# Optimization experiments

Hardware: AMD Instinct MI355X
Metric: run time of the kernel (lower is better)

The kernel has to match this reference:

```python
import jax, jax.numpy as jnp
import numpy as np

IN_F, OUT_F, GRID = 1024, 1024, 8
B = 8192
GRID_LO, GRID_HI = -1.0, 1.0


def setup_inputs() -> dict:
    key = jax.random.key(0)
    k1, k2 = jax.random.split(key)
    x = jax.random.normal(k1, (B, IN_F), dtype=jnp.float32)
    # buffers: grid is linspace expanded over in_features; sigma = 1.5*h
    h = (GRID_HI - GRID_LO) / (GRID - 1)
    grid = jnp.broadcast_to(jnp.linspace(GRID_LO, GRID_HI, GRID, dtype=jnp.float32), (IN_F, GRID))
    sigma = jnp.float32(1.5 * h)
    # params
    scale_base = jnp.ones((IN_F, OUT_F), dtype=jnp.float32)
    scale_spline = jnp.ones((IN_F, OUT_F), dtype=jnp.float32)
    # kaiming_uniform-ish init: bound = sqrt(6/fan_in)/sqrt(1+a^2) approximated by small uniform
    fan_in = IN_F * GRID
    gain = np.sqrt(2.0 / (1.0 + 5.0 * 0.1 * 0.1))
    bound = gain * np.sqrt(3.0 / fan_in)
    spline_weight = jax.random.uniform(k2, (OUT_F, IN_F, GRID), dtype=jnp.float32, minval=-bound, maxval=bound)
    return {"x": x, "scale_base": scale_base, "spline_weight": spline_weight,
            "scale_spline": scale_spline, "grid": grid, "sigma": sigma}


def reference(x, scale_base, spline_weight, scale_spline, grid, sigma):
    # x: [B, I]; grid: [I, G]; spline_weight: [O, I, G]; scales: [I, O]
    base_out = jnp.einsum('bi,io->bo', jax.nn.silu(x), scale_base)
    # RBF bases: exp(-((x - grid)/sigma)^2)  -> [B, I, G]
    bases = jnp.exp(-jnp.square((x[:, :, None] - grid[None, :, :]) / sigma))
    # fused spline contraction (mathematically identical to big,oig->bio then bio,io->bo)
    spline_out = jnp.einsum('big,oig,io->bo', bases, spline_weight, scale_spline)
    return base_out + spline_out
```

## Files before the change

kernel.cpp:

```cpp
#include <hip/hip_runtime.h>


#define BATCH 8192
#define IN_F  1024
#define OUT_F 1024
#define GRID_N 8
#define K2    (IN_F * GRID_N)
#define KTOT  (IN_F + K2)

#define BM 128
#define BN 128
#define BK 64
#define BK8 128

typedef __bf16 bf16x8 __attribute__((ext_vector_type(8)));
typedef float  f32x4  __attribute__((ext_vector_type(4)));
typedef int    int32x8 __attribute__((ext_vector_type(8)));

__device__ __forceinline__ void gl2lds16(const void* g, void* l) {
  __builtin_amdgcn_global_load_lds(
      (const __attribute__((address_space(1))) void*)g,
      (__attribute__((address_space(3))) void*)l, 16, 0, 0);
}

__device__ __forceinline__ void pack_fp8x8(const float* v, int& w0, int& w1) {
  w0 = 0; w1 = 0;
  w0 = __builtin_amdgcn_cvt_pk_fp8_f32(v[0], v[1], w0, false);
  w0 = __builtin_amdgcn_cvt_pk_fp8_f32(v[2], v[3], w0, true);
  w1 = __builtin_amdgcn_cvt_pk_fp8_f32(v[4], v[5], w1, false);
  w1 = __builtin_amdgcn_cvt_pk_fp8_f32(v[6], v[7], w1, true);
}

__global__ __launch_bounds__(256)
void kan_mix(const float* __restrict__ x, const float* __restrict__ sb,
             const float* __restrict__ sw, const float* __restrict__ ss,
             const float* __restrict__ grid, const float* __restrict__ sigma,
             __bf16* __restrict__ sbT, unsigned char* __restrict__ wbt8,
             unsigned char* __restrict__ Ab8, __bf16* __restrict__ sbA) {
  const int t = threadIdx.x;
  const int bx = blockIdx.x;
  if (bx < 256) {
    __shared__ float tile[64][65];
    const int o0 = (bx & 15) * 64, k0 = (bx >> 4) * 64;
    const int r = t >> 4, c4 = (t & 15) * 4;
    #pragma unroll
    for (int it = 0; it < 4; ++it) {
      const int k = k0 + r + it * 16;
      float4 v = *(const float4*)(sb + (size_t)k * OUT_F + o0 + c4);
      tile[r + it * 16][c4 + 0] = v.x; tile[r + it * 16][c4 + 1] = v.y;
      tile[r + it * 16][c4 + 2] = v.z; tile[r + it * 16][c4 + 3] = v.w;
    }
    __syncthreads();
    #pragma unroll
    for (int it = 0; it < 4; ++it) {
      const int ol = r + it * 16;
      union { __bf16 h[4]; uint2 q; } s;
      #pragma unroll
      for (int e = 0; e < 4; ++e) s.h[e] = (__bf16)tile[c4 + e][ol];
      *(uint2*)(sbT + (size_t)(o0 + ol) * IN_F + k0 + c4) = s.q;
    }
  } else if (bx < 512) {
    __shared__ float tile[64][65];
    const int sp = bx - 256;
    const int o0 = (sp >> 4) * 64;
    const int j0 = (sp & 15) * 512;
    const int i0 = j0 >> 3;
    const int r = t >> 4, c4 = (t & 15) * 4;
    #pragma unroll
    for (int it = 0; it < 4; ++it) {
      const int i = i0 + r + it * 16;
      float4 v = *(const float4*)(ss + (size_t)i * OUT_F + o0 + c4);
      tile[r + it * 16][c4 + 0] = v.x; tile[r + it * 16][c4 + 1] = v.y;
      tile[r + it * 16][c4 + 2] = v.z; tile[r + it * 16][c4 + 3] = v.w;
    }
    __syncthreads();
    #pragma unroll
    for (int p = 0; p < 16; ++p) {
      const int f = p * 256 + t;
      const int o_l = f >> 6, i_l = f & 63;
      const float sc = tile[i_l][o_l];
      const float* swp = sw + (size_t)(o0 + o_l) * K2 + j0 + i_l * 8;
      float4 a = *(const float4*)swp;
      float4 b = *(const float4*)(swp + 4);
      float vv[8] = {a.x * sc, a.y * sc, a.z * sc, a.w * sc,
                     b.x * sc, b.y * sc, b.z * sc, b.w * sc};
      int w0, w1; pack_fp8x8(vv, w0, w1);
      *(int2*)(wbt8 + (size_t)(o0 + o_l) * K2 + j0 + i_l * 8) = make_int2(w0, w1);
    }
  } else {
    const int b = bx - 512;
    const float inv_sigma = 1.0f / sigma[0];
    const float* xrow = x + (size_t)b * IN_F;
    unsigned char* arow = Ab8 + (size_t)b * K2;
    __bf16* srow = sbA + (size_t)b * IN_F;
    {
      float4 v = ((const float4*)xrow)[t];
      float vv[4] = {v.x, v.y, v.z, v.w};
      union { __bf16 h[4]; uint2 q; } s;
      #pragma unroll
      for (int e = 0; e < 4; ++e) s.h[e] = (__bf16)(vv[e] / (1.0f + __expf(-vv[e])));
      ((uint2*)srow)[t] = s.q;
    }
    #pragma unroll
    for (int it = 0; it < 4; ++it) {
      const int i = t + it * 256;
      const float u = xrow[i];
      float4 g0 = *(const float4*)(grid + (size_t)i * GRID_N);
      float4 g1 = *(const float4*)(grid + (size_t)i * GRID_N + 4);
      float gg[8] = {g0.x, g0.y, g0.z, g0.w, g1.x, g1.y, g1.z, g1.w};
      float bb[8];
      #pragma unroll
      for (int g = 0; g < GRID_N; ++g) {
        float d = (u - gg[g]) * inv_sigma;
        bb[g] = __expf(-d * d);
      }
      int w0, w1; pack_fp8x8(bb, w0, w1);
      *(int2*)(arow + (size_t)i * GRID_N) = make_int2(w0, w1);
    }
  }
}

__global__ __launch_bounds__(512, 2)
void kan_gemm_all(const unsigned char* __restrict__ Ab8,
                  const unsigned char* __restrict__ wbt8,
                  const __bf16* __restrict__ sbA,
                  const __bf16* __restrict__ sbT,
                  float* __restrict__ out) {
  __shared__ unsigned char smem[2][49152];

  const int tid = threadIdx.x;
  const int bx  = blockIdx.x;
  const int xcd = bx & 7, loc = bx >> 3;
  const int r0 = (xcd * 4 + (loc >> 3)) * 256;
  const int c0 = (loc & 7) * 128;

  const int lane = tid & 63, wave = tid >> 6;
  const int wm = wave & 3, wn = wave >> 2;
  const int quad = lane >> 4, l15 = lane & 15;

  int a_off8[4][2], b_off8[4][2];
  #pragma unroll
  for (int t4 = 0; t4 < 4; ++t4) {
    const int rowA = wm * 64 + t4 * 16 + l15;
    const int rowB = wn * 64 + t4 * 16 + l15;
    #pragma unroll
    for (int h = 0; h < 2; ++h) {
      a_off8[t4][h] = rowA * 128 + (((quad * 2 + h) ^ (rowA & 7)) * 16);
      b_off8[t4][h] = 32768 + rowB * 128 + (((quad * 2 + h) ^ (rowB & 7)) * 16);
    }
  }
  int a_off16[2][4], b_off16[2][4];
  #pragma unroll
  for (int ks = 0; ks < 2; ++ks) {
    const int kc = ks * 4 + quad;
    #pragma unroll
    for (int t4 = 0; t4 < 4; ++t4) {
      const int rowA = wm * 64 + t4 * 16 + l15;
      a_off16[ks][t4] = (rowA * 8 + (kc ^ (rowA & 7))) * 16;
      const int rowB = wn * 64 + t4 * 16 + l15;
      b_off16[ks][t4] = 32768 + (rowB * 8 + (kc ^ (rowB & 7))) * 16;
    }
  }

  const unsigned char* aS8[4]; const __bf16* aS16[4]; int aD[4];
  #pragma unroll
  for (int it = 0; it < 4; ++it) {
    const int p = it * 512 + tid;
    const int row = p >> 3;
    const int kc  = (p & 7) ^ (row & 7);
    aS8[it]  = Ab8 + (size_t)(r0 + row) * K2 + kc * 16;
    aS16[it] = sbA + (size_t)(r0 + row) * IN_F + kc * 8;
    aD[it] = p * 16;
  }
  const unsigned char* bS8[2]; const __bf16* bS16[2]; int bD[2];
  #pragma unroll
  for (int it = 0; it < 2; ++it) {
    const int q = it * 512 + tid;
    const int row = q >> 3;
    const int kc  = (q & 7) ^ (row & 7);
    bS8[it]  = wbt8 + (size_t)(c0 + row) * K2 + kc * 16;
    bS16[it] = sbT + (size_t)(c0 + row) * IN_F + kc * 8;
    bD[it] = 32768 + q * 16;
  }

  f32x4 zero; zero[0] = 0.f; zero[1] = 0.f; zero[2] = 0.f; zero[3] = 0.f;
  f32x4 acc[4][4];
  #pragma unroll
  for (int a = 0; a < 4; ++a)
    #pragma unroll
    for (int b = 0; b < 4; ++b) acc[a][b] = zero;

  #pragma unroll
  for (int it = 0; it < 4; ++it) gl2lds16(aS8[it], &smem[0][aD[it]]);
  #pragma unroll
  for (int it = 0; it < 2; ++it) gl2lds16(bS8[it], &smem[0][bD[it]]);
  __syncthreads();

  int cur = 0;
  for (int t = 0; t < 64; ++t) {
    const int nxt = cur ^ 1;
    if (t < 63) {
      const int kb = (t + 1) * BK8;
      #pragma unroll
      for (int it = 0; it < 4; ++it) gl2lds16(aS8[it] + kb, &smem[nxt][aD[it]]);
      #pragma unroll
      for (int it = 0; it < 2; ++it) gl2lds16(bS8[it] + kb, &smem[nxt][bD[it]]);
    } else {
      #pragma unroll
      for (int it = 0; it < 4; ++it) gl2lds16(aS16[it], &smem[nxt][aD[it]]);
      #pragma unroll
      for (int it = 0; it < 2; ++it) gl2lds16(bS16[it], &smem[nxt][bD[it]]);
    }
    const unsigned char* sp = smem[cur];
    union frag { int32x8 v; uint4 q[2]; };
    frag af[4], bfv[4];
    #pragma unroll
    for (int t4 = 0; t4 < 4; ++t4) {
      af[t4].q[0]  = *(const uint4*)(sp + a_off8[t4][0]);
      af[t4].q[1]  = *(const uint4*)(sp + a_off8[t4][1]);
      bfv[t4].q[0] = *(const uint4*)(sp + b_off8[t4][0]);
      bfv[t4].q[1] = *(const uint4*)(sp + b_off8[t4][1]);
    }
    __builtin_amdgcn_s_setprio(1);
    #pragma unroll
    for (int tm = 0; tm < 4; ++tm)
      #pragma unroll
      for (int tn = 0; tn < 4; ++tn)
        acc[tm][tn] = __builtin_amdgcn_mfma_scale_f32_16x16x128_f8f6f4(
            af[tm].v, bfv[tn].v, acc[tm][tn],
            0, 0, 0, 0x7F7F7F7F, 0, 0x7F7F7F7F);
    __builtin_amdgcn_s_setprio(0);
    __syncthreads();
    cur = nxt;
  }

  for (int t = 0; t < 16; ++t) {
    const int nxt = cur ^ 1;
    if (t < 15) {
      const int ke = (t + 1) * BK;
      #pragma unroll
      for (int it = 0; it < 4; ++it) gl2lds16(aS16[it] + ke, &smem[nxt][aD[it]]);
      #pragma unroll
      for (int it = 0; it < 2; ++it) gl2lds16(bS16[it] + ke, &smem[nxt][bD[it]]);
    }
    const unsigned char* sp = smem[cur];
    #pragma unroll
    for (int ks = 0; ks < 2; ++ks) {
      bf16x8 af[4], bfv[4];
      #pragma unroll
      for (int t4 = 0; t4 < 4; ++t4) af[t4]  = *(const bf16x8*)(sp + a_off16[ks][t4]);
      #pragma unroll
      for (int t4 = 0; t4 < 4; ++t4) bfv[t4] = *(const bf16x8*)(sp + b_off16[ks][t4]);
      __builtin_amdgcn_s_setprio(1);
      #pragma unroll
      for (int tm = 0; tm < 4; ++tm)
        #pragma unroll
        for (int tn = 0; tn < 4; ++tn)
          acc[tm][tn] = __builtin_amdgcn_mfma_f32_16x16x32_bf16(
              af[tm], bfv[tn], acc[tm][tn], 0, 0, 0);
      __builtin_amdgcn_s_setprio(0);
    }
    __syncthreads();
    cur = nxt;
  }

  #pragma unroll
  for (int tm = 0; tm < 4; ++tm) {
    const int row = r0 + wm * 64 + tm * 16 + quad * 4;
    #pragma unroll
    for (int tn = 0; tn < 4; ++tn) {
      const int col = c0 + wn * 64 + tn * 16 + l15;
      float* op = out + (size_t)row * OUT_F + col;
      #pragma unroll
      for (int r = 0; r < 4; ++r)
        op[(size_t)r * OUT_F] = acc[tm][tn][r];
    }
  }
}

__global__ __launch_bounds__(256)
void kan_prep_w_full(const float* __restrict__ sb, const float* __restrict__ sw,
                     const float* __restrict__ ss, __bf16* __restrict__ wbt) {
  const int t = threadIdx.x;
  if (blockIdx.x < 256) {
    __shared__ float tile[64][65];
    const int o0 = (blockIdx.x & 15) * 64, k0 = (blockIdx.x >> 4) * 64;
    const int r = t >> 4, c4 = (t & 15) * 4;
    #pragma unroll
    for (int it = 0; it < 4; ++it) {
      const int k = k0 + r + it * 16;
      float4 v = *(const float4*)(sb + (size_t)k * OUT_F + o0 + c4);
      tile[r + it * 16][c4 + 0] = v.x; tile[r + it * 16][c4 + 1] = v.y;
      tile[r + it * 16][c4 + 2] = v.z; tile[r + it * 16][c4 + 3] = v.w;
    }
    __syncthreads();
    #pragma unroll
    for (int it = 0; it < 4; ++it) {
      const int ol = r + it * 16;
      union { __bf16 h[4]; uint2 q; } s;
      #pragma unroll
      for (int e = 0; e < 4; ++e) s.h[e] = (__bf16)tile[c4 + e][ol];
      *(uint2*)(wbt + (size_t)(o0 + ol) * KTOT + k0 + c4) = s.q;
    }
  } else {
    const size_t e = ((size_t)(blockIdx.x - 256) * 256 + t) * 8;
    const int o = (int)(e >> 13);
    const int j = (int)(e & 8191);
    const int i = j >> 3;
    const float sc = ss[(size_t)i * OUT_F + o];
    float4 a = *(const float4*)(sw + e);
    float4 b = *(const float4*)(sw + e + 4);
    float vv[8] = {a.x, a.y, a.z, a.w, b.x, b.y, b.z, b.w};
    union { __bf16 h[8]; uint4 q; } s;
    #pragma unroll
    for (int g = 0; g < 8; ++g) s.h[g] = (__bf16)(vv[g] * sc);
    *(uint4*)(wbt + (size_t)o * KTOT + IN_F + j) = s.q;
  }
}

__global__ __launch_bounds__(256, 2)
void kan_gemm_fused(const float* __restrict__ x, const __bf16* __restrict__ wbt,
                    const float* __restrict__ grid, const float* __restrict__ sigma,
                    float* __restrict__ out) {
  __shared__ __bf16 As[BM * BK];
  __shared__ __bf16 Bs[BN * BK];
  __shared__ float  gLds[IN_F * GRID_N];
  const int tid = threadIdx.x;
  const int bx  = blockIdx.x;
  const int c0  = (bx & 7) * BN;
  const int r0  = (bx >> 3) * BM;
  for (int idx = tid; idx < IN_F * GRID_N / 4; idx += 256)
    ((float4*)gLds)[idx] = ((const float4*)grid)[idx];
  const float inv_sigma = 1.0f / sigma[0];
  const int lane = tid & 63, wave = tid >> 6;
  const int wm = wave & 1, wn = wave >> 1;
  const int quad = lane >> 4, l15 = lane & 15;
  f32x4 zero; zero[0] = 0.f; zero[1] = 0.f; zero[2] = 0.f; zero[3] = 0.f;
  f32x4 acc[4][4];
  #pragma unroll
  for (int a = 0; a < 4; ++a)
    #pragma unroll
    for (int b = 0; b < 4; ++b) acc[a][b] = zero;
  const int m = tid >> 1, half = tid & 1;
  const float* xrow = x + (size_t)(r0 + m) * IN_F;
  __syncthreads();
  for (int kb = 0; kb < KTOT; kb += BK) {
    union { __bf16 h[32]; uint4 q[4]; } av;
    if (kb < IN_F) {
      const float4* xp = (const float4*)(xrow + kb + half * 32);
      #pragma unroll
      for (int j4 = 0; j4 < 8; ++j4) {
        float4 v = xp[j4];
        float vv[4] = {v.x, v.y, v.z, v.w};
        #pragma unroll
        for (int e = 0; e < 4; ++e)
          av.h[j4 * 4 + e] = (__bf16)(vv[e] / (1.0f + __expf(-vv[e])));
      }
    } else {
      const int i0 = (kb - IN_F) >> 3;
      float4 xv = *(const float4*)(xrow + i0 + half * 4);
      float xs[4] = {xv.x, xv.y, xv.z, xv.w};
      #pragma unroll
      for (int ii = 0; ii < 4; ++ii) {
        const float u = xs[ii];
        const float* gp = &gLds[(i0 + half * 4 + ii) * GRID_N];
        #pragma unroll
        for (int g = 0; g < GRID_N; ++g) {
          float d = (u - gp[g]) * inv_sigma;
          av.h[ii * 8 + g] = (__bf16)__expf(-d * d);
        }
      }
    }
    __syncthreads();
    {
      uint4* dst = (uint4*)&As[m * BK + half * 32];
      #pragma unroll
      for (int qd = 0; qd < 4; ++qd) dst[qd] = av.q[qd];
    }
    #pragma unroll
    for (int it = 0; it < 4; ++it) {
      const int idx = it * 2048 + tid * 8;
      const int n = idx >> 6, k = idx & 63;
      gl2lds16(wbt + (size_t)(c0 + n) * KTOT + kb + k, &Bs[idx]);
    }
    __syncthreads();
    #pragma unroll
    for (int ks = 0; ks < 2; ++ks) {
      bf16x8 af[4], bfv[4];
      #pragma unroll
      for (int t4 = 0; t4 < 4; ++t4)
        af[t4] = *(const bf16x8*)&As[(wm * 64 + t4 * 16 + l15) * BK + ks * 32 + quad * 8];
      #pragma unroll
      for (int t4 = 0; t4 < 4; ++t4)
        bfv[t4] = *(const bf16x8*)&Bs[(wn * 64 + t4 * 16 + l15) * BK + ks * 32 + quad * 8];
      #pragma unroll
      for (int tm = 0; tm < 4; ++tm)
        #pragma unroll
        for (int tn = 0; tn < 4; ++tn)
          acc[tm][tn] = __builtin_amdgcn_mfma_f32_16x16x32_bf16(
              af[tm], bfv[tn], acc[tm][tn], 0, 0, 0);
    }
  }
  #pragma unroll
  for (int tm = 0; tm < 4; ++tm) {
    const int row = r0 + wm * 64 + tm * 16 + quad * 4;
    #pragma unroll
    for (int tn = 0; tn < 4; ++tn) {
      const int col = c0 + wn * 64 + tn * 16 + l15;
      float* op = out + (size_t)row * OUT_F + col;
      #pragma unroll
      for (int r = 0; r < 4; ++r)
        op[(size_t)r * OUT_F] = acc[tm][tn][r];
    }
  }
}

extern "C" void kernel_launch(void* const* d_in, const int* in_sizes, int n_in,
                              void* d_out, int out_size, void* d_ws, size_t ws_size,
                              hipStream_t stream) {
  const float* x     = (const float*)d_in[0];
  const float* sb    = (const float*)d_in[1];
  const float* sw    = (const float*)d_in[2];
  const float* ss    = (const float*)d_in[3];
  const float* grid  = (const float*)d_in[4];
  const float* sigma = (const float*)d_in[5];
  float* out = (float*)d_out;

  const size_t SBT_BYTES = (size_t)OUT_F * IN_F * 2;
  const size_t WS_BYTES  = (size_t)OUT_F * K2;
  const size_t A_BYTES   = (size_t)BATCH * K2;
  const size_t SBA_BYTES = (size_t)BATCH * IN_F * 2;

  if (ws_size >= SBT_BYTES + WS_BYTES + A_BYTES + SBA_BYTES) {
    __bf16*        sbT  = (__bf16*)d_ws;
    unsigned char* wbt8 = (unsigned char*)d_ws + SBT_BYTES;
    unsigned char* Ab8  = (unsigned char*)d_ws + SBT_BYTES + WS_BYTES;
    __bf16*        sbA  = (__bf16*)((char*)d_ws + SBT_BYTES + WS_BYTES + A_BYTES);
    kan_mix<<<dim3(512 + BATCH), dim3(256), 0, stream>>>(
        x, sb, sw, ss, grid, sigma, sbT, wbt8, Ab8, sbA);
    kan_gemm_all<<<dim3((BATCH / 256) * (OUT_F / 128)), dim3(512), 0, stream>>>(
        Ab8, wbt8, sbA, sbT, out);
  } else {
    __bf16* wbt = (__bf16*)d_ws;
    kan_prep_w_full<<<dim3(4352), dim3(256), 0, stream>>>(sb, sw, ss, wbt);
    kan_gemm_fused<<<dim3((BATCH / BM) * (OUT_F / BN)), dim3(256), 0, stream>>>(
        x, wbt, grid, sigma, out);
  }
}
```

Measured before the change: 244.3 us.

## Restructure GEMM main loop into ping-pong phases with two-ahead prefetch

Rewrites the fp8 and bf16 GEMM loops of kan_gemm_all so each k-step is split into four quadrant phases. LDS fragment reads, MFMA groups and async global-to-LDS loads for tile t+2 are interleaved, separated by explicit s_barriers and sched_barriers, and the wait is a partial vmcnt instead of a full __syncthreads drain. The aim is to keep MFMA issue overlapped with LDS reads and the global prefetch, and to avoid stalls on loads that are still in flight. The cost is tighter manual ordering: stores into the buffer being read depend on barrier placement, and there are more barriers per iteration.

```diff
diff --git a/kernel.cpp b/kernel.cpp
--- a/kernel.cpp
+++ b/kernel.cpp
@@ -13,6 +13,10 @@
 #define BK 64
 #define BK8 128
 
+#define GBM 256
+#define GBN 128
+#define SLOT 49152
+
 typedef __bf16 bf16x8 __attribute__((ext_vector_type(8)));
 typedef float  f32x4  __attribute__((ext_vector_type(4)));
 typedef int    int32x8 __attribute__((ext_vector_type(8)));
@@ -30,6 +34,14 @@
   w1 = __builtin_amdgcn_cvt_pk_fp8_f32(v[4], v[5], w1, false);
   w1 = __builtin_amdgcn_cvt_pk_fp8_f32(v[6], v[7], w1, true);
 }
+
+#define KBAR() do { __builtin_amdgcn_sched_barrier(0); \
+    asm volatile("" ::: "memory"); \
+    __builtin_amdgcn_s_barrier(); \
+    asm volatile("" ::: "memory"); } while (0)
+
+#define MFMA8(d, A, B) d = __builtin_amdgcn_mfma_scale_f32_16x16x128_f8f6f4( \
+    (A).v, (B).v, d, 0, 0, 0, 0x7F7F7F7F, 0, 0x7F7F7F7F)
 
 __global__ __launch_bounds__(256)
 void kan_mix(const float* __restrict__ x, const float* __restrict__ sb,
@@ -126,13 +138,14 @@
                   const __bf16* __restrict__ sbA,
                   const __bf16* __restrict__ sbT,
                   float* __restrict__ out) {
-  __shared__ unsigned char smem[2][49152];
+  __shared__ unsigned char smem[2][SLOT];
+  unsigned char* smem0 = &smem[0][0];
 
   const int tid = threadIdx.x;
   const int bx  = blockIdx.x;
-  const int xcd = bx & 7, loc = bx >> 3;
-  const int r0 = (xcd * 4 + (loc >> 3)) * 256;
-  const int c0 = (loc & 7) * 128;
+  const int xcd = bx & 7, j = bx >> 3;
+  const int r0 = (xcd * 4 + (j >> 3)) * GBM;
+  const int c0 = (j & 7) * GBN;
 
   const int lane = tid & 63, wave = tid >> 6;
   const int wm = wave & 3, wn = wave >> 2;
@@ -162,26 +175,49 @@
     }
   }
 
-  const unsigned char* aS8[4]; const __bf16* aS16[4]; int aD[4];
+  const unsigned char* aSrc8[4]; const __bf16* aSrc16[4]; int dstA[4];
   #pragma unroll
   for (int it = 0; it < 4; ++it) {
     const int p = it * 512 + tid;
     const int row = p >> 3;
     const int kc  = (p & 7) ^ (row & 7);
-    aS8[it]  = Ab8 + (size_t)(r0 + row) * K2 + kc * 16;
-    aS16[it] = sbA + (size_t)(r0 + row) * IN_F + kc * 8;
-    aD[it] = p * 16;
-  }
-  const unsigned char* bS8[2]; const __bf16* bS16[2]; int bD[2];
+    aSrc8[it]  = Ab8 + (size_t)(r0 + row) * K2 + kc * 16;
+    aSrc16[it] = sbA + (size_t)(r0 + row) * IN_F + kc * 8;
+    dstA[it] = p * 16;
+  }
+  const unsigned char* bSrc8[2]; const __bf16* bSrc16[2]; int dstB[2];
   #pragma unroll
   for (int it = 0; it < 2; ++it) {
     const int q = it * 512 + tid;
     const int row = q >> 3;
     const int kc  = (q & 7) ^ (row & 7);
-    bS8[it]  = wbt8 + (size_t)(c0 + row) * K2 + kc * 16;
-    bS16[it] = sbT + (size_t)(c0 + row) * IN_F + kc * 8;
-    bD[it] = 32768 + q * 16;
-  }
+    bSrc8[it]  = wbt8 + (size_t)(c0 + row) * K2 + kc * 16;
+    bSrc16[it] = sbT + (size_t)(c0 + row) * IN_F + kc * 8;
+    dstB[it] = 32768 + q * 16;
+  }
+
+  auto stageB = [&](unsigned char* base, int g) {
+    if (g < 64) {
+      const size_t off = (size_t)g * BK8;
+      #pragma unroll
+      for (int it = 0; it < 2; ++it) gl2lds16(bSrc8[it] + off, base + dstB[it]);
+    } else {
+      const size_t off = (size_t)(g - 64) * BK;
+      #pragma unroll
+      for (int it = 0; it < 2; ++it) gl2lds16(bSrc16[it] + off, base + dstB[it]);
+    }
+  };
+  auto stageA = [&](unsigned char* base, int g) {
+    if (g < 64) {
+      const size_t off = (size_t)g * BK8;
+      #pragma unroll
+      for (int it = 0; it < 4; ++it) gl2lds16(aSrc8[it] + off, base + dstA[it]);
+    } else {
+      const size_t off = (size_t)(g - 64) * BK;
+      #pragma unroll
+      for (int it = 0; it < 4; ++it) gl2lds16(aSrc16[it] + off, base + dstA[it]);
+    }
+  };
 
   f32x4 zero; zero[0] = 0.f; zero[1] = 0.f; zero[2] = 0.f; zero[3] = 0.f;
   f32x4 acc[4][4];
@@ -190,78 +226,133 @@
     #pragma unroll
     for (int b = 0; b < 4; ++b) acc[a][b] = zero;
 
-  #pragma unroll
-  for (int it = 0; it < 4; ++it) gl2lds16(aS8[it], &smem[0][aD[it]]);
-  #pragma unroll
-  for (int it = 0; it < 2; ++it) gl2lds16(bS8[it], &smem[0][bD[it]]);
-  __syncthreads();
-
-  int cur = 0;
+  stageB(smem0, 0); stageA(smem0, 0);
+  stageB(smem0 + SLOT, 1); stageA(smem0 + SLOT, 1);
+  asm volatile("s_waitcnt vmcnt(6)" ::: "memory");
+  __builtin_amdgcn_s_barrier();
+  asm volatile("" ::: "memory");
+
+  union frag { int32x8 v; uint4 q[2]; };
+  #pragma unroll 2
   for (int t = 0; t < 64; ++t) {
-    const int nxt = cur ^ 1;
-    if (t < 63) {
-      const int kb = (t + 1) * BK8;
-      #pragma unroll
-      for (int it = 0; it < 4; ++it) gl2lds16(aS8[it] + kb, &smem[nxt][aD[it]]);
-      #pragma unroll
-      for (int it = 0; it < 2; ++it) gl2lds16(bS8[it] + kb, &smem[nxt][bD[it]]);
-    } else {
-      #pragma unroll
-      for (int it = 0; it < 4; ++it) gl2lds16(aS16[it], &smem[nxt][aD[it]]);
-      #pragma unroll
-      for (int it = 0; it < 2; ++it) gl2lds16(bS16[it], &smem[nxt][bD[it]]);
-    }
-    const unsigned char* sp = smem[cur];
-    union frag { int32x8 v; uint4 q[2]; };
-    frag af[4], bfv[4];
-    #pragma unroll
-    for (int t4 = 0; t4 < 4; ++t4) {
-      af[t4].q[0]  = *(const uint4*)(sp + a_off8[t4][0]);
-      af[t4].q[1]  = *(const uint4*)(sp + a_off8[t4][1]);
-      bfv[t4].q[0] = *(const uint4*)(sp + b_off8[t4][0]);
-      bfv[t4].q[1] = *(const uint4*)(sp + b_off8[t4][1]);
-    }
-    __builtin_amdgcn_s_setprio(1);
-    #pragma unroll
-    for (int tm = 0; tm < 4; ++tm)
-      #pragma unroll
-      for (int tn = 0; tn < 4; ++tn)
-        acc[tm][tn] = __builtin_amdgcn_mfma_scale_f32_16x16x128_f8f6f4(
-            af[tm].v, bfv[tn].v, acc[tm][tn],
-            0, 0, 0, 0x7F7F7F7F, 0, 0x7F7F7F7F);
-    __builtin_amdgcn_s_setprio(0);
-    __syncthreads();
-    cur = nxt;
-  }
-
+    unsigned char* sp = smem0 + (t & 1) * SLOT;
+    const int t2 = t + 2;
+    frag af0, af1, af2, af3, bf0, bf1, bf2, bf3;
+    af0.q[0] = *(const uint4*)(sp + a_off8[0][0]);
+    af0.q[1] = *(const uint4*)(sp + a_off8[0][1]);
+    af1.q[0] = *(const uint4*)(sp + a_off8[1][0]);
+    af1.q[1] = *(const uint4*)(sp + a_off8[1][1]);
+    bf0.q[0] = *(const uint4*)(sp + b_off8[0][0]);
+    bf0.q[1] = *(const uint4*)(sp + b_off8[0][1]);
+    bf1.q[0] = *(const uint4*)(sp + b_off8[1][0]);
+    bf1.q[1] = *(const uint4*)(sp + b_off8[1][1]);
+    KBAR();
+    __builtin_amdgcn_s_setprio(1);
+    MFMA8(acc[0][0], af0, bf0); MFMA8(acc[0][1], af0, bf1);
+    MFMA8(acc[1][0], af1, bf0); MFMA8(acc[1][1], af1, bf1);
+    __builtin_amdgcn_s_setprio(0);
+    KBAR();
+    bf2.q[0] = *(const uint4*)(sp + b_off8[2][0]);
+    bf2.q[1] = *(const uint4*)(sp + b_off8[2][1]);
+    bf3.q[0] = *(const uint4*)(sp + b_off8[3][0]);
+    bf3.q[1] = *(const uint4*)(sp + b_off8[3][1]);
+    KBAR();
+    __builtin_amdgcn_s_setprio(1);
+    MFMA8(acc[0][2], af0, bf2); MFMA8(acc[0][3], af0, bf3);
+    MFMA8(acc[1][2], af1, bf2); MFMA8(acc[1][3], af1, bf3);
+    __builtin_amdgcn_s_setprio(0);
+    KBAR();
+    af2.q[0] = *(const uint4*)(sp + a_off8[2][0]);
+    af2.q[1] = *(const uint4*)(sp + a_off8[2][1]);
+    af3.q[0] = *(const uint4*)(sp + a_off8[3][0]);
+    af3.q[1] = *(const uint4*)(sp + a_off8[3][1]);
+    stageB(sp, t2);
+    KBAR();
+    __builtin_amdgcn_s_setprio(1);
+    MFMA8(acc[2][0], af2, bf0); MFMA8(acc[2][1], af2, bf1);
+    MFMA8(acc[3][0], af3, bf0); MFMA8(acc[3][1], af3, bf1);
+    __builtin_amdgcn_s_setprio(0);
+    KBAR();
+    stageA(sp, t2);
+    KBAR();
+    __builtin_amdgcn_s_setprio(1);
+    MFMA8(acc[2][2], af2, bf2); MFMA8(acc[2][3], af2, bf3);
+    MFMA8(acc[3][2], af3, bf2); MFMA8(acc[3][3], af3, bf3);
+    __builtin_amdgcn_s_setprio(0);
+    asm volatile("s_waitcnt vmcnt(6)" ::: "memory");
+    KBAR();
+  }
+
+  #pragma unroll 2
   for (int t = 0; t < 16; ++t) {
-    const int nxt = cur ^ 1;
-    if (t < 15) {
-      const int ke = (t + 1) * BK;
-      #pragma unroll
-      for (int it = 0; it < 4; ++it) gl2lds16(aS16[it] + ke, &smem[nxt][aD[it]]);
-      #pragma unroll
-      for (int it = 0; it < 2; ++it) gl2lds16(bS16[it] + ke, &smem[nxt][bD[it]]);
-    }
-    const unsigned char* sp = smem[cur];
-    #pragma unroll
-    for (int ks = 0; ks < 2; ++ks) {
-      bf16x8 af[4], bfv[4];
-      #pragma unroll
-      for (int t4 = 0; t4 < 4; ++t4) af[t4]  = *(const bf16x8*)(sp + a_off16[ks][t4]);
-      #pragma unroll
-      for (int t4 = 0; t4 < 4; ++t4) bfv[t4] = *(const bf16x8*)(sp + b_off16[ks][t4]);
-      __builtin_amdgcn_s_setprio(1);
-      #pragma unroll
-      for (int tm = 0; tm < 4; ++tm)
-        #pragma unroll
-        for (int tn = 0; tn < 4; ++tn)
-          acc[tm][tn] = __builtin_amdgcn_mfma_f32_16x16x32_bf16(
-              af[tm], bfv[tn], acc[tm][tn], 0, 0, 0);
-      __builtin_amdgcn_s_setprio(0);
-    }
-    __syncthreads();
-    cur = nxt;
+    unsigned char* sp = smem0 + (t & 1) * SLOT;
+    const int t2 = t + 2;
+    bf16x8 afv[2][2], bfv[2][4];
+    #pragma unroll
+    for (int ks = 0; ks < 2; ++ks) {
+      afv[ks][0] = *(const bf16x8*)(sp + a_off16[ks][0]);
+      afv[ks][1] = *(const bf16x8*)(sp + a_off16[ks][1]);
+      bfv[ks][0] = *(const bf16x8*)(sp + b_off16[ks][0]);
+      bfv[ks][1] = *(const bf16x8*)(sp + b_off16[ks][1]);
+    }
+    KBAR();
+    __builtin_amdgcn_s_setprio(1);
+    #pragma unroll
+    for (int ks = 0; ks < 2; ++ks) {
+      acc[0][0] = __builtin_amdgcn_mfma_f32_16x16x32_bf16(afv[ks][0], bfv[ks][0], acc[0][0], 0, 0, 0);
+      acc[0][1] = __builtin_amdgcn_mfma_f32_16x16x32_bf16(afv[ks][0], bfv[ks][1], acc[0][1], 0, 0, 0);
+      acc[1][0] = __builtin_amdgcn_mfma_f32_16x16x32_bf16(afv[ks][1], bfv[ks][0], acc[1][0], 0, 0, 0);
+      acc[1][1] = __builtin_amdgcn_mfma_f32_16x16x32_bf16(afv[ks][1], bfv[ks][1], acc[1][1], 0, 0, 0);
+    }
+    __builtin_amdgcn_s_setprio(0);
+    KBAR();
+    #pragma unroll
+    for (int ks = 0; ks < 2; ++ks) {
+      bfv[ks][2] = *(const bf16x8*)(sp + b_off16[ks][2]);
+      bfv[ks][3] = *(const bf16x8*)(sp + b_off16[ks][3]);
+    }
+    KBAR();
+    __builtin_amdgcn_s_setprio(1);
+    #pragma unroll
+    for (int ks = 0; ks < 2; ++ks) {
+      acc[0][2] = __builtin_amdgcn_mfma_f32_16x16x32_bf16(afv[ks][0], bfv[ks][2], acc[0][2], 0, 0, 0);
+      acc[0][3] = __builtin_amdgcn_mfma_f32_16x16x32_bf16(afv[ks][0], bfv[ks][3], acc[0][3], 0, 0, 0);
+      acc[1][2] = __builtin_amdgcn_mfma_f32_16x16x32_bf16(afv[ks][1], bfv[ks][2], acc[1][2], 0, 0, 0);
+      acc[1][3] = __builtin_amdgcn_mfma_f32_16x16x32_bf16(afv[ks][1], bfv[ks][3], acc[1][3], 0, 0, 0);
+    }
+    __builtin_amdgcn_s_setprio(0);
+    KBAR();
+    #pragma unroll
+    for (int ks = 0; ks < 2; ++ks) {
+      afv[ks][0] = *(const bf16x8*)(sp + a_off16[ks][2]);
+      afv[ks][1] = *(const bf16x8*)(sp + a_off16[ks][3]);
+    }
+    if (t < 14) stageB(sp, 64 + t2);
+    KBAR();
+    __builtin_amdgcn_s_setprio(1);
+    #pragma unroll
+    for (int ks = 0; ks < 2; ++ks) {
+      acc[2][0] = __builtin_amdgcn_mfma_f32_16x16x32_bf16(afv[ks][0], bfv[ks][0], acc[2][0], 0, 0, 0);
+      acc[2][1] = __builtin_amdgcn_mfma_f32_16x16x32_bf16(afv[ks][0], bfv[ks][1], acc[2][1], 0, 0, 0);
+      acc[3][0] = __builtin_amdgcn_mfma_f32_16x16x32_bf16(afv[ks][1], bfv[ks][0], acc[3][0], 0, 0, 0);
+      acc[3][1] = __builtin_amdgcn_mfma_f32_16x16x32_bf16(afv[ks][1], bfv[ks][1], acc[3][1], 0, 0, 0);
+    }
+    __builtin_amdgcn_s_setprio(0);
+    KBAR();
+    if (t < 14) stageA(sp, 64 + t2);
+    KBAR();
+    __builtin_amdgcn_s_setprio(1);
+    #pragma unroll
+    for (int ks = 0; ks < 2; ++ks) {
+      acc[2][2] = __builtin_amdgcn_mfma_f32_16x16x32_bf16(afv[ks][0], bfv[ks][2], acc[2][2], 0, 0, 0);
+      acc[2][3] = __builtin_amdgcn_mfma_f32_16x16x32_bf16(afv[ks][0], bfv[ks][3], acc[2][3], 0, 0, 0);
+      acc[3][2] = __builtin_amdgcn_mfma_f32_16x16x32_bf16(afv[ks][1], bfv[ks][2], acc[3][2], 0, 0, 0);
+      acc[3][3] = __builtin_amdgcn_mfma_f32_16x16x32_bf16(afv[ks][1], bfv[ks][3], acc[3][3], 0, 0, 0);
+    }
+    __builtin_amdgcn_s_setprio(0);
+    if (t < 14) { asm volatile("s_waitcnt vmcnt(6)" ::: "memory"); }
+    else        { asm volatile("s_waitcnt vmcnt(0)" ::: "memory"); }
+    KBAR();
   }
 
   #pragma unroll
@@ -438,7 +529,7 @@
     __bf16*        sbA  = (__bf16*)((char*)d_ws + SBT_BYTES + WS_BYTES + A_BYTES);
     kan_mix<<<dim3(512 + BATCH), dim3(256), 0, stream>>>(
         x, sb, sw, ss, grid, sigma, sbT, wbt8, Ab8, sbA);
-    kan_gemm_all<<<dim3((BATCH / 256) * (OUT_F / 128)), dim3(512), 0, stream>>>(
+    kan_gemm_all<<<dim3((BATCH / GBM) * (OUT_F / GBN)), dim3(512), 0, stream>>>(
         Ab8, wbt8, sbA, sbT, out);
   } else {
     __bf16* wbt = (__bf16*)d_ws;
```

Result: no change. 242.9 us (-0.6%).
